# Performance work log

Measured on AMD Instinct MI355X. Metric: run time of the kernel, lower is better.

Reference implementation:

```python
import jax, jax.numpy as jnp
import numpy as np

N = 20000      # nodes
E = 320000     # edges per relation
D = 128        # d_model
H = 2          # attention heads


def _gat(x, src, dst, W, al, ar, b):
    """DGL-style GATConv on a single relation (same src/dst node type).
    x: [N, in], W: [in, H*O], al/ar: [H, O], b: [H*O]. Returns [N, H, O]."""
    h, o = al.shape
    feat = (x @ W).reshape(N, h, o)                 # [N, H, O]
    el = jnp.sum(feat * al, axis=-1)                # [N, H]
    er = jnp.sum(feat * ar, axis=-1)                # [N, H]
    e = jax.nn.leaky_relu(el[src] + er[dst], 0.2)   # [E, H] per-edge logits
    m = jax.ops.segment_max(e, dst, num_segments=N)            # per-dst max
    ee = jnp.exp(e - m[dst])
    s = jax.ops.segment_sum(ee, dst, num_segments=N)
    alpha = ee / jnp.maximum(s[dst], 1e-9)          # edge softmax over incoming edges
    out = jax.ops.segment_sum(alpha[:, :, None] * feat[src], dst, num_segments=N)
    return out + b.reshape(1, h, o)


def setup_inputs() -> dict:
    key = jax.random.key(0)
    ks = jax.random.split(key, 24)
    d = {
        'x': jax.random.normal(ks[0], (N, D), jnp.float32),
        'src0': jax.random.randint(ks[1], (E,), 0, N, jnp.int32),
        'dst0': jax.random.randint(ks[2], (E,), 0, N, jnp.int32),
        'src1': jax.random.randint(ks[3], (E,), 0, N, jnp.int32),
        'dst1': jax.random.randint(ks[4], (E,), 0, N, jnp.int32),
    }
    sc = 0.1
    # layer 1: in=D, out per head=2D, heads=H
    d['W1_0'] = jax.random.normal(ks[5], (D, H * 2 * D), jnp.float32) * sc
    d['al1_0'] = jax.random.normal(ks[6], (H, 2 * D), jnp.float32) * sc
    d['ar1_0'] = jax.random.normal(ks[7], (H, 2 * D), jnp.float32) * sc
    d['b1_0'] = jnp.zeros((H * 2 * D,), jnp.float32)
    d['W1_1'] = jax.random.normal(ks[8], (D, H * 2 * D), jnp.float32) * sc
    d['al1_1'] = jax.random.normal(ks[9], (H, 2 * D), jnp.float32) * sc
    d['ar1_1'] = jax.random.normal(ks[10], (H, 2 * D), jnp.float32) * sc
    d['b1_1'] = jnp.zeros((H * 2 * D,), jnp.float32)
    # layer 2: in=2D, out per head=D, heads=H
    d['W2_0'] = jax.random.normal(ks[11], (2 * D, H * D), jnp.float32) * sc
    d['al2_0'] = jax.random.normal(ks[12], (H, D), jnp.float32) * sc
    d['ar2_0'] = jax.random.normal(ks[13], (H, D), jnp.float32) * sc
    d['b2_0'] = jnp.zeros((H * D,), jnp.float32)
    d['W2_1'] = jax.random.normal(ks[14], (2 * D, H * D), jnp.float32) * sc
    d['al2_1'] = jax.random.normal(ks[15], (H, D), jnp.float32) * sc
    d['ar2_1'] = jax.random.normal(ks[16], (H, D), jnp.float32) * sc
    d['b2_1'] = jnp.zeros((H * D,), jnp.float32)
    return d


def reference(x, src0, dst0, src1, dst1,
              W1_0, al1_0, ar1_0, b1_0, W1_1, al1_1, ar1_1, b1_1,
              W2_0, al2_0, ar2_0, b2_0, W2_1, al2_1, ar2_1, b2_1):
    # conv1: HeteroGraphConv sum over relations, then mean over heads, relu
    h1 = _gat(x, src0, dst0, W1_0, al1_0, ar1_0, b1_0) \
       + _gat(x, src1, dst1, W1_1, al1_1, ar1_1, b1_1)   # [N, H, 2D]
    h1 = jax.nn.relu(h1.mean(axis=1))                    # [N, 2D]; dropout is eval-mode identity
    # conv2: same structure, then mean over heads
    h2 = _gat(h1, src0, dst0, W2_0, al2_0, ar2_0, b2_0) \
       + _gat(h1, src1, dst1, W2_1, al2_1, ar2_1, b2_1)  # [N, H, D]
    return h2.mean(axis=1)                                # [N, D]
```

## Files before the change

kernel.cpp:

```cpp
#include <hip/hip_runtime.h>


#define NN 20000
#define NE 320000

typedef unsigned short bf16_t;
typedef __attribute__((ext_vector_type(8))) short short8;
typedef __attribute__((ext_vector_type(4))) float f32x4;

__device__ __forceinline__ float bf2f(bf16_t u) {
    return __uint_as_float(((unsigned)u) << 16);
}
__device__ __forceinline__ bf16_t f2bf(float f) {
    unsigned x = __float_as_uint(f);
    unsigned r = (x + 0x7fffu + ((x >> 16) & 1u)) >> 16;
    return (bf16_t)r;
}
__device__ __forceinline__ unsigned pk2bf(float a, float b) {
    return (unsigned)f2bf(a) | ((unsigned)f2bf(b) << 16);
}
__device__ __forceinline__ float lrelu(float v) {
    return (v > 0.f) ? v : 0.2f * v;
}
__device__ __forceinline__ void load_x2(const void* x, int flag, int idx,
                                        float& v0, float& v1) {
    if (flag) {
        float2 f = ((const float2*)x)[idx];
        v0 = f.x; v1 = f.y;
    } else {
        unsigned pk = ((const unsigned*)x)[idx];
        v0 = bf2f((bf16_t)(pk & 0xffffu));
        v1 = bf2f((bf16_t)(pk >> 16));
    }
}

#define NTC 16
struct CzArgs {
    const void* src[NTC];
    bf16_t* dst[NTC];
    int n[NTC];
    int nblk[NTC + 1];
    int* zero_ptr;
    int zn;
    const unsigned* xsrc;
    int* flag_out;
};
__global__ void convzero_kernel(CzArgs a) {
    __shared__ int fl_s;
    int t = threadIdx.x;
    if (t < 64) {
        float mx = 0.f;
        for (int i = t; i < 256; i += 64) {
            float v = fabsf(bf2f((bf16_t)(a.xsrc[i] & 0xffffu)));
            v = (v <= 1e30f) ? v : 1e30f;
            mx = fmaxf(mx, v);
        }
        for (int off = 32; off > 0; off >>= 1) mx = fmaxf(mx, __shfl_xor(mx, off));
        if (t == 0) {
            int f = (mx > 1e6f) ? 1 : 0;
            fl_s = f;
            if (blockIdx.x == 0) *a.flag_out = f;
        }
    }
    __syncthreads();
    int flag = fl_s;
    int b = blockIdx.x;
    int ti = 0;
#pragma unroll 1
    for (; ti <= NTC; ++ti) {
        if (b < a.nblk[ti]) break;
        b -= a.nblk[ti];
    }
    int i = b * 256 + t;
    if (ti < NTC) {
        if (i < a.n[ti]) {
            if (flag) a.dst[ti][i] = f2bf(((const float*)a.src[ti])[i]);
            else      a.dst[ti][i] = ((const bf16_t*)a.src[ti])[i];
        }
    } else {
        if (i < a.zn) a.zero_ptr[i] = 0;
    }
}

struct PrepArgs {
    const bf16_t *W1[2], *W2[2];
    const bf16_t *al1[2], *ar1[2], *al2[2], *ar2[2];
    const bf16_t *b1[2], *b2[2];
    float *wal1, *war1;
    float *wal2, *war2;
    float *bc1, *bc2;
    bf16_t *Wc1f;
    bf16_t *Wzf;
};
__device__ __forceinline__ void prep_body(const PrepArgs& p, int bx, int tid) {
    if (bx < 4) {
        int t = bx * 256 + tid;
        int lr = t >> 9, rel = (t >> 8) & 1, h = (t >> 7) & 1, k = t & 127;
        const bf16_t* av = lr ? p.ar1[rel] : p.al1[rel];
        const bf16_t* W = p.W1[rel];
        float s = 0.f;
        for (int o = 0; o < 256; ++o)
            s += bf2f(W[k * 512 + h * 256 + o]) * bf2f(av[h * 256 + o]);
        (lr ? p.war1 : p.wal1)[(rel * 2 + h) * 128 + k] = s;
    } else if (bx < 12) {
        int t = (bx - 4) * 256 + tid;
        int lr = t >> 10, rel = (t >> 9) & 1, h = (t >> 8) & 1, k = t & 255;
        const bf16_t* av = lr ? p.ar2[rel] : p.al2[rel];
        const bf16_t* W = p.W2[rel];
        float s = 0.f;
        for (int o = 0; o < 128; ++o)
            s += bf2f(W[k * 256 + h * 128 + o]) * bf2f(av[h * 128 + o]);
        (lr ? p.war2 : p.wal2)[(rel * 2 + h) * 256 + k] = s;
    } else if (bx < 14) {
        int t = (bx - 12) * 256 + tid;
        if (t < 256) {
            p.bc1[t] = 0.5f * (bf2f(p.b1[0][t]) + bf2f(p.b1[0][256 + t]) +
                               bf2f(p.b1[1][t]) + bf2f(p.b1[1][256 + t]));
        } else if (t < 384) {
            int o = t - 256;
            p.bc2[o] = 0.5f * (bf2f(p.b2[0][o]) + bf2f(p.b2[0][128 + o]) +
                               bf2f(p.b2[1][o]) + bf2f(p.b2[1][128 + o]));
        }
    } else if (bx < 78) {
        int i = (bx - 14) * 256 + tid;
        int lane = i & 63;
        int t2 = i >> 6;
        int ct = t2 >> 4, ks = t2 & 15;
        int col = ct * 16 + (lane & 15);
        bf16_t* out = p.Wc1f + (size_t)i * 8;
#pragma unroll
        for (int j = 0; j < 8; ++j) {
            int r = ks * 32 + ((lane >> 4) << 3) + j;
            int rel = r >> 8, h = (r >> 7) & 1, kx = r & 127;
            out[j] = f2bf(0.5f * bf2f(p.W1[rel][kx * 512 + h * 256 + col]));
        }
    } else {
        int b = bx - 78;
        int rel = b >> 5;
        int i = (b & 31) * 256 + tid;
        int lane = i & 63;
        int t2 = i >> 6;
        int ct = t2 >> 3, ks = t2 & 7;
        int col = ct * 16 + (lane & 15);
        bf16_t* out = p.Wzf + (size_t)rel * 65536 + (size_t)i * 8;
#pragma unroll
        for (int j = 0; j < 8; ++j) {
            int r = ks * 32 + ((lane >> 4) << 3) + j;
            out[j] = f2bf(0.5f * bf2f(p.W2[rel][r * 256 + col]));
        }
    }
}

struct Csr2 {
    const int* src[2];
    const int* dst[2];
    int* cnt[2];
    int* offs[2];
    int* rank[2];
    int* srcc[2];
};
struct PhArgs { PrepArgs p; Csr2 c; };
__global__ void prep_hist_kernel(PhArgs a) {
    int bx = blockIdx.x;
    if (bx < 142) {
        prep_body(a.p, bx, threadIdx.x);
    } else {
        int b = bx - 142;
        int rel = b / 1250;
        int i = (b - rel * 1250) * 256 + threadIdx.x;
        if (i < NE)
            a.c.rank[rel][i] = atomicAdd(&a.c.cnt[rel][a.c.dst[rel][i]], 1);
    }
}

__global__ void scan2_kernel(Csr2 c, int n) {
    int rel = blockIdx.x;
    const int* cnt = c.cnt[rel];
    int* offs = c.offs[rel];
    __shared__ int sums[256];
    int t = threadIdx.x;
    int chunk = (n + 255) >> 8;
    int lo = t * chunk;
    int hi = min(lo + chunk, n);
    int s = 0;
    for (int i = lo; i < hi; ++i) s += cnt[i];
    sums[t] = s;
    __syncthreads();
    if (t == 0) {
        int run = 0;
        for (int i = 0; i < 256; ++i) { int v = sums[i]; sums[i] = run; run += v; }
    }
    __syncthreads();
    int run = sums[t];
    for (int i = lo; i < hi; ++i) { int v = cnt[i]; offs[i] = run; run += v; }
    if (t == 255) offs[n] = run;
}

__global__ void scat_elr_kernel(Csr2 c, const void* __restrict__ x,
                                const int* __restrict__ flagp,
                                const float* __restrict__ wal1,
                                const float* __restrict__ war1,
                                float* __restrict__ el0, float* __restrict__ er0,
                                float* __restrict__ el1, float* __restrict__ er1) {
    __shared__ float wl[512], wr[512];
    int t = threadIdx.x;
    if (blockIdx.x < 5000) {
        wl[t] = wal1[t]; wl[t + 256] = wal1[t + 256];
        wr[t] = war1[t]; wr[t + 256] = war1[t + 256];
        __syncthreads();
        int fl = *flagp;
        int w = t >> 6, lane = t & 63;
        int node = blockIdx.x * 4 + w;
        float v0, v1;
        load_x2(x, fl, node * 64 + lane, v0, v1);
        float de[4], dr[4];
#pragma unroll
        for (int cch = 0; cch < 4; ++cch) {
            de[cch] = v0 * wl[cch * 128 + 2 * lane] + v1 * wl[cch * 128 + 2 * lane + 1];
            dr[cch] = v0 * wr[cch * 128 + 2 * lane] + v1 * wr[cch * 128 + 2 * lane + 1];
        }
#pragma unroll
        for (int off = 32; off > 0; off >>= 1) {
#pragma unroll
            for (int cch = 0; cch < 4; ++cch) {
                de[cch] += __shfl_xor(de[cch], off);
                dr[cch] += __shfl_xor(dr[cch], off);
            }
        }
        if (lane == 0) {
            el0[node * 2 + 0] = de[0]; el0[node * 2 + 1] = de[1];
            el1[node * 2 + 0] = de[2]; el1[node * 2 + 1] = de[3];
            er0[node * 2 + 0] = dr[0]; er0[node * 2 + 1] = dr[1];
            er1[node * 2 + 0] = dr[2]; er1[node * 2 + 1] = dr[3];
        }
    } else {
        int b = blockIdx.x - 5000;
        int rel = b / 313;
        int base = (b - rel * 313) * 1024 + t * 4;
        const int* dstp = c.dst[rel];
        const int* srcp = c.src[rel];
        const int* rkp  = c.rank[rel];
        const int* offp = c.offs[rel];
        int* sc = c.srcc[rel];
        if (base + 3 < NE) {
            int4 dv = *(const int4*)(dstp + base);
            int4 rv = *(const int4*)(rkp + base);
            int4 sv = *(const int4*)(srcp + base);
            sc[offp[dv.x] + rv.x] = sv.x;
            sc[offp[dv.y] + rv.y] = sv.y;
            sc[offp[dv.z] + rv.z] = sv.z;
            sc[offp[dv.w] + rv.w] = sv.w;
        } else {
            for (int k = 0; k < 4 && base + k < NE; ++k)
                sc[offp[dstp[base + k]] + rkp[base + k]] = srcp[base + k];
        }
    }
}

__device__ __forceinline__ void wave_softmax(
    const int* __restrict__ srcc, int beg, int deg,
    const float* __restrict__ el, float er_h0, float er_h1, int lane,
    int& sreg, float& a0, float& a1,
    float& m0, float& i0, float& m1, float& i1) {
    float mm0 = -1e30f, ss0 = 0.f, mm1 = -1e30f, ss1 = 0.f;
    float e0r = 0.f, e1r = 0.f;
    sreg = 0;
    for (int j = lane; j < deg; j += 64) {
        int s = srcc[beg + j];
        float2 ev = ((const float2*)el)[s];
        float e0 = lrelu(ev.x + er_h0);
        float e1 = lrelu(ev.y + er_h1);
        if (j < 64) { sreg = s; e0r = e0; e1r = e1; }
        float mn0 = fmaxf(mm0, e0);
        ss0 = ss0 * __expf(mm0 - mn0) + __expf(e0 - mn0);
        mm0 = mn0;
        float mn1 = fmaxf(mm1, e1);
        ss1 = ss1 * __expf(mm1 - mn1) + __expf(e1 - mn1);
        mm1 = mn1;
    }
#pragma unroll
    for (int off = 1; off < 64; off <<= 1) {
        float om = __shfl_xor(mm0, off), os = __shfl_xor(ss0, off);
        float mn = fmaxf(mm0, om);
        ss0 = ss0 * __expf(mm0 - mn) + os * __expf(om - mn);
        mm0 = mn;
        om = __shfl_xor(mm1, off); os = __shfl_xor(ss1, off);
        mn = fmaxf(mm1, om);
        ss1 = ss1 * __expf(mm1 - mn) + os * __expf(om - mn);
        mm1 = mn;
    }
    m0 = mm0; m1 = mm1;
    i0 = 1.f / fmaxf(ss0, 1e-9f);
    i1 = 1.f / fmaxf(ss1, 1e-9f);
    a0 = __expf(e0r - m0) * i0;
    a1 = __expf(e1r - m1) * i1;
}

__global__ void agg1_kernel(
    const int* __restrict__ offs0, const int* __restrict__ srcc0,
    const float* __restrict__ el0, const float* __restrict__ er0,
    const int* __restrict__ offs1, const int* __restrict__ srcc1,
    const float* __restrict__ el1, const float* __restrict__ er1,
    const void* __restrict__ x, const int* __restrict__ flagp,
    bf16_t* __restrict__ y1) {
    int t = threadIdx.x;
    int w = t >> 6, lane = t & 63;
    int slot = lane >> 5, m = lane & 31;
    int d = blockIdx.x * 4 + w;
    int beg0 = offs0[d], deg0 = offs0[d + 1] - beg0;
    int beg1 = offs1[d], deg1 = offs1[d + 1] - beg1;
    float er00 = er0[d * 2], er01 = er0[d * 2 + 1];
    float er10 = er1[d * 2], er11 = er1[d * 2 + 1];
    int fl = *flagp;

    int sr0, sr1;
    float a00, a01, a10, a11;
    float m00, i00, m01, i01, m10, i10, m11, i11;
    wave_softmax(srcc0, beg0, deg0, el0, er00, er01, lane, sr0, a00, a01, m00, i00, m01, i01);
    wave_softmax(srcc1, beg1, deg1, el1, er10, er11, lane, sr1, a10, a11, m10, i10, m11, i11);

    auto xload = [&](int s, float v[4]) {
        if (fl) {
            float4 f = ((const float4*)x)[s * 32 + m];
            v[0] = f.x; v[1] = f.y; v[2] = f.z; v[3] = f.w;
        } else {
            uint2 pk = ((const uint2*)x)[s * 32 + m];
            v[0] = bf2f((bf16_t)(pk.x & 0xffffu));
            v[1] = bf2f((bf16_t)(pk.x >> 16));
            v[2] = bf2f((bf16_t)(pk.y & 0xffffu));
            v[3] = bf2f((bf16_t)(pk.y >> 16));
        }
    };
    float h0[4] = {}, h1[4] = {};
    float g0[4] = {}, g1[4] = {};
    {
        int dm = min(deg0, 64);
        int T = (dm + 3) & ~3;
        for (int jj = slot; jj < T; jj += 4) {
            int j2 = jj + 2;
            int sA = __shfl(sr0, jj), sB = __shfl(sr0, j2);
            float pA0 = __shfl(a00, jj), pA1 = __shfl(a01, jj);
            float pB0 = __shfl(a00, j2), pB1 = __shfl(a01, j2);
            if (jj >= dm) { sA = 0; pA0 = 0.f; pA1 = 0.f; }
            if (j2 >= dm) { sB = 0; pB0 = 0.f; pB1 = 0.f; }
            float vA[4], vB[4];
            xload(sA, vA);
            xload(sB, vB);
#pragma unroll
            for (int k = 0; k < 4; ++k) {
                h0[k] += pA0 * vA[k] + pB0 * vB[k];
                h1[k] += pA1 * vA[k] + pB1 * vB[k];
            }
        }
        for (int jj = 64 + slot; jj < deg0; jj += 2) {
            int sA = srcc0[beg0 + jj];
            float2 ev = ((const float2*)el0)[sA];
            float pA0 = __expf(lrelu(ev.x + er00) - m00) * i00;
            float pA1 = __expf(lrelu(ev.y + er01) - m01) * i01;
            float vA[4];
            xload(sA, vA);
#pragma unroll
            for (int k = 0; k < 4; ++k) {
                h0[k] += pA0 * vA[k];
                h1[k] += pA1 * vA[k];
            }
        }
    }
    {
        int dm = min(deg1, 64);
        int T = (dm + 3) & ~3;
        for (int jj = slot; jj < T; jj += 4) {
            int j2 = jj + 2;
            int sA = __shfl(sr1, jj), sB = __shfl(sr1, j2);
            float pA0 = __shfl(a10, jj), pA1 = __shfl(a11, jj);
            float pB0 = __shfl(a10, j2), pB1 = __shfl(a11, j2);
            if (jj >= dm) { sA = 0; pA0 = 0.f; pA1 = 0.f; }
            if (j2 >= dm) { sB = 0; pB0 = 0.f; pB1 = 0.f; }
            float vA[4], vB[4];
            xload(sA, vA);
            xload(sB, vB);
#pragma unroll
            for (int k = 0; k < 4; ++k) {
                g0[k] += pA0 * vA[k] + pB0 * vB[k];
                g1[k] += pA1 * vA[k] + pB1 * vB[k];
            }
        }
        for (int jj = 64 + slot; jj < deg1; jj += 2) {
            int sA = srcc1[beg1 + jj];
            float2 ev = ((const float2*)el1)[sA];
            float pA0 = __expf(lrelu(ev.x + er10) - m10) * i10;
            float pA1 = __expf(lrelu(ev.y + er11) - m11) * i11;
            float vA[4];
            xload(sA, vA);
#pragma unroll
            for (int k = 0; k < 4; ++k) {
                g0[k] += pA0 * vA[k];
                g1[k] += pA1 * vA[k];
            }
        }
    }
#pragma unroll
    for (int k = 0; k < 4; ++k) {
        h0[k] += __shfl_xor(h0[k], 32);
        h1[k] += __shfl_xor(h1[k], 32);
        g0[k] += __shfl_xor(g0[k], 32);
        g1[k] += __shfl_xor(g1[k], 32);
    }
    if (slot == 0) {
        bf16_t* yr = y1 + (size_t)d * 512;
        uint2 u;
        u.x = pk2bf(h0[0], h0[1]); u.y = pk2bf(h0[2], h0[3]);
        ((uint2*)yr)[m] = u;
        u.x = pk2bf(h1[0], h1[1]); u.y = pk2bf(h1[2], h1[3]);
        ((uint2*)(yr + 128))[m] = u;
        u.x = pk2bf(g0[0], g0[1]); u.y = pk2bf(g0[2], g0[3]);
        ((uint2*)(yr + 256))[m] = u;
        u.x = pk2bf(g1[0], g1[1]); u.y = pk2bf(g1[2], g1[3]);
        ((uint2*)(yr + 384))[m] = u;
    }
}

__global__ void gemm1_kernel(const bf16_t* __restrict__ A, const bf16_t* __restrict__ Wf,
                             const float* __restrict__ bc1, bf16_t* __restrict__ h1,
                             const float* __restrict__ wal2, const float* __restrict__ war2,
                             float* __restrict__ el2_0, float* __restrict__ er2_0,
                             float* __restrict__ el2_1, float* __restrict__ er2_1,
                             int n) {
    constexpr int K = 512, M = 256, KS = 16, NF = 8;
    int w = threadIdx.x >> 6, lane = threadIdx.x & 63;
    int q = lane >> 4, m16 = lane & 15;
    int rf = blockIdx.y * 64 + w * 16;
    if (rf >= n) return;
    f32x4 acc[NF] = {};
    const bf16_t* Arow = A + (size_t)(rf + m16) * K + q * 8;
    for (int ks = 0; ks < KS; ++ks) {
        short8 af = *(const short8*)(Arow + ks * 32);
#pragma unroll
        for (int f = 0; f < NF; ++f) {
            int ct = blockIdx.x * NF + f;
            short8 bfr = *(const short8*)(Wf + ((size_t)(ct * KS + ks) * 64 + lane) * 8);
            acc[f] = __builtin_amdgcn_mfma_f32_16x16x32_bf16(af, bfr, acc[f], 0, 0, 0);
        }
    }
    int col0 = blockIdx.x * (NF * 16);
    float del[2][2][4] = {};
    float der[2][2][4] = {};
#pragma unroll
    for (int f = 0; f < NF; ++f) {
        int col = col0 + f * 16 + m16;
        float bcv = bc1[col];
        float wle[2][2], wre[2][2];
#pragma unroll
        for (int rel = 0; rel < 2; ++rel)
#pragma unroll
            for (int h = 0; h < 2; ++h) {
                wle[rel][h] = wal2[(rel * 2 + h) * 256 + col];
                wre[rel][h] = war2[(rel * 2 + h) * 256 + col];
            }
#pragma unroll
        for (int r = 0; r < 4; ++r) {
            int row = rf + q * 4 + r;
            float v = fmaxf(acc[f][r] + bcv, 0.f);
            bf16_t hb = f2bf(v);
            h1[(size_t)row * M + col] = hb;
            float vb = bf2f(hb);
#pragma unroll
            for (int rel = 0; rel < 2; ++rel)
#pragma unroll
                for (int h = 0; h < 2; ++h) {
                    del[rel][h][r] += vb * wle[rel][h];
                    der[rel][h][r] += vb * wre[rel][h];
                }
        }
    }
#pragma unroll
    for (int off = 1; off < 16; off <<= 1) {
#pragma unroll
        for (int rel = 0; rel < 2; ++rel)
#pragma unroll
            for (int h = 0; h < 2; ++h)
#pragma unroll
                for (int r = 0; r < 4; ++r) {
                    del[rel][h][r] += __shfl_xor(del[rel][h][r], off);
                    der[rel][h][r] += __shfl_xor(der[rel][h][r], off);
                }
    }
    if (m16 == 0) {
#pragma unroll
        for (int r = 0; r < 4; ++r) {
            int row = rf + q * 4 + r;
            atomicAdd(&el2_0[row * 2 + 0], del[0][0][r]);
            atomicAdd(&el2_0[row * 2 + 1], del[0][1][r]);
            atomicAdd(&el2_1[row * 2 + 0], del[1][0][r]);
            atomicAdd(&el2_1[row * 2 + 1], del[1][1][r]);
            atomicAdd(&er2_0[row * 2 + 0], der[0][0][r]);
            atomicAdd(&er2_0[row * 2 + 1], der[0][1][r]);
            atomicAdd(&er2_1[row * 2 + 0], der[1][0][r]);
            atomicAdd(&er2_1[row * 2 + 1], der[1][1][r]);
        }
    }
}

__global__ void gemmz_kernel(const bf16_t* __restrict__ A, const bf16_t* __restrict__ Wzf,
                             bf16_t* __restrict__ z, int n) {
    constexpr int K = 256, M = 256, KS = 8, NF = 8;
    int rel = blockIdx.z;
    const bf16_t* Wf = Wzf + (size_t)rel * 65536;
    bf16_t* C = z + (size_t)rel * NN * 256;
    int w = threadIdx.x >> 6, lane = threadIdx.x & 63;
    int q = lane >> 4, m16 = lane & 15;
    int rf = blockIdx.y * 64 + w * 16;
    if (rf >= n) return;
    f32x4 acc[NF] = {};
    const bf16_t* Arow = A + (size_t)(rf + m16) * K + q * 8;
    for (int ks = 0; ks < KS; ++ks) {
        short8 af = *(const short8*)(Arow + ks * 32);
#pragma unroll
        for (int f = 0; f < NF; ++f) {
            int ct = blockIdx.x * NF + f;
            short8 bfr = *(const short8*)(Wf + ((size_t)(ct * KS + ks) * 64 + lane) * 8);
            acc[f] = __builtin_amdgcn_mfma_f32_16x16x32_bf16(af, bfr, acc[f], 0, 0, 0);
        }
    }
    int col0 = blockIdx.x * (NF * 16);
#pragma unroll
    for (int f = 0; f < NF; ++f) {
#pragma unroll
        for (int r = 0; r < 4; ++r) {
            int row = rf + q * 4 + r;
            C[(size_t)row * M + col0 + f * 16 + m16] = f2bf(acc[f][r]);
        }
    }
}

__global__ void aggout_kernel(
    const int* __restrict__ offs0, const int* __restrict__ srcc0,
    const float* __restrict__ el0, const float* __restrict__ er0,
    const int* __restrict__ offs1, const int* __restrict__ srcc1,
    const float* __restrict__ el1, const float* __restrict__ er1,
    const bf16_t* __restrict__ z, const float* __restrict__ bc2,
    void* __restrict__ out, const int* __restrict__ flagp) {
    int t = threadIdx.x;
    int w = t >> 6, lane = t & 63;
    int slot = lane >> 5, m = lane & 31;
    int h = m >> 4;
    int d = blockIdx.x * 4 + w;
    int beg0 = offs0[d], deg0 = offs0[d + 1] - beg0;
    int beg1 = offs1[d], deg1 = offs1[d + 1] - beg1;
    float er00 = er0[d * 2], er01 = er0[d * 2 + 1];
    float er10 = er1[d * 2], er11 = er1[d * 2 + 1];

    int sr0, sr1;
    float a00, a01, a10, a11;
    float m00, i00, m01, i01, m10, i10, m11, i11;
    wave_softmax(srcc0, beg0, deg0, el0, er00, er01, lane, sr0, a00, a01, m00, i00, m01, i01);
    wave_softmax(srcc1, beg1, deg1, el1, er10, er11, lane, sr1, a10, a11, m10, i10, m11, i11);

    float acc[8] = {};
    auto fmadd8 = [&](float a, uint4 p) {
        acc[0] += a * bf2f((bf16_t)(p.x & 0xffffu));
        acc[1] += a * bf2f((bf16_t)(p.x >> 16));
        acc[2] += a * bf2f((bf16_t)(p.y & 0xffffu));
        acc[3] += a * bf2f((bf16_t)(p.y >> 16));
        acc[4] += a * bf2f((bf16_t)(p.z & 0xffffu));
        acc[5] += a * bf2f((bf16_t)(p.z >> 16));
        acc[6] += a * bf2f((bf16_t)(p.w & 0xffffu));
        acc[7] += a * bf2f((bf16_t)(p.w >> 16));
    };
    {
        const uint4* zp = (const uint4*)z;
        int dm = min(deg0, 64);
        int T = (dm + 3) & ~3;
        for (int jj = slot; jj < T; jj += 4) {
            int j2 = jj + 2;
            int sA = __shfl(sr0, jj), sB = __shfl(sr0, j2);
            float xA0 = __shfl(a00, jj), xA1 = __shfl(a01, jj);
            float xB0 = __shfl(a00, j2), xB1 = __shfl(a01, j2);
            float aA = h ? xA1 : xA0;
            float aB = h ? xB1 : xB0;
            if (jj >= dm) { sA = 0; aA = 0.f; }
            if (j2 >= dm) { sB = 0; aB = 0.f; }
            uint4 pA = zp[sA * 32 + m];
            uint4 pB = zp[sB * 32 + m];
            fmadd8(aA, pA);
            fmadd8(aB, pB);
        }
        for (int jj = 64 + slot; jj < deg0; jj += 2) {
            int sA = srcc0[beg0 + jj];
            float2 ev = ((const float2*)el0)[sA];
            float aA = h ? (__expf(lrelu(ev.y + er01) - m01) * i01)
                         : (__expf(lrelu(ev.x + er00) - m00) * i00);
            uint4 pA = zp[sA * 32 + m];
            fmadd8(aA, pA);
        }
    }
    {
        const uint4* zp = (const uint4*)(z + (size_t)NN * 256);
        int dm = min(deg1, 64);
        int T = (dm + 3) & ~3;
        for (int jj = slot; jj < T; jj += 4) {
            int j2 = jj + 2;
            int sA = __shfl(sr1, jj), sB = __shfl(sr1, j2);
            float xA0 = __shfl(a10, jj), xA1 = __shfl(a11, jj);
            float xB0 = __shfl(a10, j2), xB1 = __shfl(a11, j2);
            float aA = h ? xA1 : xA0;
            float aB = h ? xB1 : xB0;
            if (jj >= dm) { sA = 0; aA = 0.f; }
            if (j2 >= dm) { sB = 0; aB = 0.f; }
            uint4 pA = zp[sA * 32 + m];
            uint4 pB = zp[sB * 32 + m];
            fmadd8(aA, pA);
            fmadd8(aB, pB);
        }
        for (int jj = 64 + slot; jj < deg1; jj += 2) {
            int sA = srcc1[beg1 + jj];
            float2 ev = ((const float2*)el1)[sA];
            float aA = h ? (__expf(lrelu(ev.y + er11) - m11) * i11)
                         : (__expf(lrelu(ev.x + er10) - m10) * i10);
            uint4 pA = zp[sA * 32 + m];
            fmadd8(aA, pA);
        }
    }
#pragma unroll
    for (int k = 0; k < 8; ++k) acc[k] += __shfl_xor(acc[k], 32);
#pragma unroll
    for (int k = 0; k < 8; ++k) acc[k] += __shfl_xor(acc[k], 16);
    if (slot == 0 && m < 16) {
        float4 b0 = ((const float4*)bc2)[m * 2];
        float4 b1 = ((const float4*)bc2)[m * 2 + 1];
        float o0 = acc[0] + b0.x, o1 = acc[1] + b0.y;
        float o2 = acc[2] + b0.z, o3 = acc[3] + b0.w;
        float o4 = acc[4] + b1.x, o5 = acc[5] + b1.y;
        float o6 = acc[6] + b1.z, o7 = acc[7] + b1.w;
        if (*flagp) {
            float4* op = (float4*)out + (size_t)d * 32 + m * 2;
            op[0] = make_float4(o0, o1, o2, o3);
            op[1] = make_float4(o4, o5, o6, o7);
        } else {
            uint4 u;
            u.x = pk2bf(o0, o1); u.y = pk2bf(o2, o3);
            u.z = pk2bf(o4, o5); u.w = pk2bf(o6, o7);
            ((uint4*)out)[(size_t)d * 16 + m] = u;
        }
    }
}

extern "C" void kernel_launch(void* const* d_in, const int* in_sizes, int n_in,
                              void* d_out, int out_size, void* d_ws, size_t ws_size,
                              hipStream_t stream) {
    (void)in_sizes; (void)n_in; (void)out_size; (void)ws_size;
    const void* x0 = d_in[0];
    const int* src0 = (const int*)d_in[1];
    const int* dst0 = (const int*)d_in[2];
    const int* src1 = (const int*)d_in[3];
    const int* dst1 = (const int*)d_in[4];

    char* ws = (char*)d_ws;
    size_t off = 0;
    auto alloc = [&](size_t bytes) -> void* {
        void* p = ws + off;
        off = (off + bytes + 255) & ~(size_t)255;
        return p;
    };
    int* flag = (int*)alloc(4);
    static const int tn[NTC] = {128 * 512, 512, 512, 512,
                                128 * 512, 512, 512, 512,
                                256 * 256, 256, 256, 256,
                                256 * 256, 256, 256, 256};
    bf16_t* tb[NTC];
    for (int i = 0; i < NTC; ++i) tb[i] = (bf16_t*)alloc((size_t)tn[i] * 2);

    bf16_t* Wc1f = (bf16_t*)alloc((size_t)512 * 256 * 2);
    bf16_t* Wzf  = (bf16_t*)alloc((size_t)2 * 65536 * 2);
    float* wal1 = (float*)alloc(512 * 4);
    float* war1 = (float*)alloc(512 * 4);
    float* wal2 = (float*)alloc(1024 * 4);
    float* war2 = (float*)alloc(1024 * 4);
    float* bc1  = (float*)alloc(256 * 4);
    float* bc2  = (float*)alloc(128 * 4);

    char* zbeg = ws + off;
    int* cnt0 = (int*)alloc(NN * 4);
    int* cnt1 = (int*)alloc(NN * 4);
    float* el2_0 = (float*)alloc(NN * 2 * 4);
    float* er2_0 = (float*)alloc(NN * 2 * 4);
    float* el2_1 = (float*)alloc(NN * 2 * 4);
    float* er2_1 = (float*)alloc(NN * 2 * 4);
    char* zend = ws + off;
    int zcount = (int)((zend - zbeg) >> 2);

    int* offs0 = (int*)alloc((NN + 1) * 4);
    int* offs1 = (int*)alloc((NN + 1) * 4);
    int* rank0 = (int*)alloc(NE * 4);
    int* rank1 = (int*)alloc(NE * 4);
    int* srcc0 = (int*)alloc(NE * 4);
    int* srcc1 = (int*)alloc(NE * 4);
    float* el1_0 = (float*)alloc(NN * 2 * 4);
    float* er1_0 = (float*)alloc(NN * 2 * 4);
    float* el1_1 = (float*)alloc(NN * 2 * 4);
    float* er1_1 = (float*)alloc(NN * 2 * 4);
    bf16_t* h1 = (bf16_t*)alloc((size_t)NN * 256 * 2);
    bf16_t* Y  = (bf16_t*)alloc((size_t)NN * 1024 * 2);
    bf16_t* y1 = Y;
    bf16_t* z  = Y;

    CzArgs cz;
    static const int din_idx[NTC] = {5, 6, 7, 8, 9, 10, 11, 12,
                                     13, 14, 15, 16, 17, 18, 19, 20};
    int total_blocks = 0;
    for (int i = 0; i < NTC; ++i) {
        cz.src[i] = d_in[din_idx[i]];
        cz.dst[i] = tb[i];
        cz.n[i] = tn[i];
        cz.nblk[i] = (tn[i] + 255) / 256;
        total_blocks += cz.nblk[i];
    }
    cz.zero_ptr = (int*)zbeg;
    cz.zn = zcount;
    cz.nblk[NTC] = (zcount + 255) / 256;
    total_blocks += cz.nblk[NTC];
    cz.xsrc = (const unsigned*)x0;
    cz.flag_out = flag;
    convzero_kernel<<<total_blocks, 256, 0, stream>>>(cz);

    PhArgs ph;
    ph.p.W1[0] = tb[0];  ph.p.W1[1] = tb[4];
    ph.p.W2[0] = tb[8];  ph.p.W2[1] = tb[12];
    ph.p.al1[0] = tb[1]; ph.p.ar1[0] = tb[2];
    ph.p.al1[1] = tb[5]; ph.p.ar1[1] = tb[6];
    ph.p.al2[0] = tb[9]; ph.p.ar2[0] = tb[10];
    ph.p.al2[1] = tb[13]; ph.p.ar2[1] = tb[14];
    ph.p.b1[0] = tb[3];  ph.p.b1[1] = tb[7];
    ph.p.b2[0] = tb[11]; ph.p.b2[1] = tb[15];
    ph.p.wal1 = wal1; ph.p.war1 = war1;
    ph.p.wal2 = wal2; ph.p.war2 = war2;
    ph.p.bc1 = bc1; ph.p.bc2 = bc2;
    ph.p.Wc1f = Wc1f; ph.p.Wzf = Wzf;
    ph.c.src[0] = src0; ph.c.src[1] = src1;
    ph.c.dst[0] = dst0; ph.c.dst[1] = dst1;
    ph.c.cnt[0] = cnt0; ph.c.cnt[1] = cnt1;
    ph.c.offs[0] = offs0; ph.c.offs[1] = offs1;
    ph.c.rank[0] = rank0; ph.c.rank[1] = rank1;
    ph.c.srcc[0] = srcc0; ph.c.srcc[1] = srcc1;
    prep_hist_kernel<<<142 + 2500, 256, 0, stream>>>(ph);

    scan2_kernel<<<2, 256, 0, stream>>>(ph.c, NN);

    scat_elr_kernel<<<5000 + 626, 256, 0, stream>>>(
        ph.c, x0, flag, wal1, war1, el1_0, er1_0, el1_1, er1_1);

    agg1_kernel<<<5000, 256, 0, stream>>>(offs0, srcc0, el1_0, er1_0,
                                          offs1, srcc1, el1_1, er1_1, x0, flag, y1);

    gemm1_kernel<<<dim3(2, 313), 256, 0, stream>>>(
        y1, Wc1f, bc1, h1, wal2, war2, el2_0, er2_0, el2_1, er2_1, NN);

    gemmz_kernel<<<dim3(2, 313, 2), 256, 0, stream>>>(h1, Wzf, z, NN);

    aggout_kernel<<<5000, 256, 0, stream>>>(offs0, srcc0, el2_0, er2_0,
                                            offs1, srcc1, el2_1, er2_1,
                                            z, bc2, d_out, flag);
}
```

Baseline: 323.1 us.

## Split per-node aggregation across relations into separate waves

In both aggregation kernels, each wave now handles one (node, relation) pair instead of one node covering both relations. The grids double, so there are twice as many waves and each runs a shorter serial chain of softmax and gather loops. In aggout the two relation partial sums are combined through shared memory with a block barrier before the bias add and store. This trades extra shared-memory traffic and a sync for more parallelism and latency hiding, and the duplicated per-relation code goes away.

```diff
diff --git a/kernel.cpp b/kernel.cpp
--- a/kernel.cpp
+++ b/kernel.cpp
@@ -306,18 +306,19 @@
     int t = threadIdx.x;
     int w = t >> 6, lane = t & 63;
     int slot = lane >> 5, m = lane & 31;
-    int d = blockIdx.x * 4 + w;
-    int beg0 = offs0[d], deg0 = offs0[d + 1] - beg0;
-    int beg1 = offs1[d], deg1 = offs1[d + 1] - beg1;
-    float er00 = er0[d * 2], er01 = er0[d * 2 + 1];
-    float er10 = er1[d * 2], er11 = er1[d * 2 + 1];
+    int d = blockIdx.x * 2 + (w >> 1);
+    int rel = w & 1;
+    const int* offs = rel ? offs1 : offs0;
+    const int* srcc = rel ? srcc1 : srcc0;
+    const float* el = rel ? el1 : el0;
+    const float* er = rel ? er1 : er0;
+    int beg = offs[d], deg = offs[d + 1] - beg;
+    float erh0 = er[d * 2], erh1 = er[d * 2 + 1];
     int fl = *flagp;
 
-    int sr0, sr1;
-    float a00, a01, a10, a11;
-    float m00, i00, m01, i01, m10, i10, m11, i11;
-    wave_softmax(srcc0, beg0, deg0, el0, er00, er01, lane, sr0, a00, a01, m00, i00, m01, i01);
-    wave_softmax(srcc1, beg1, deg1, el1, er10, er11, lane, sr1, a10, a11, m10, i10, m11, i11);
+    int sr;
+    float a0, a1, m0, i0, m1, i1;
+    wave_softmax(srcc, beg, deg, el, erh0, erh1, lane, sr, a0, a1, m0, i0, m1, i1);
 
     auto xload = [&](int s, float v[4]) {
         if (fl) {
@@ -332,15 +333,14 @@
         }
     };
     float h0[4] = {}, h1[4] = {};
-    float g0[4] = {}, g1[4] = {};
     {
-        int dm = min(deg0, 64);
+        int dm = min(deg, 64);
         int T = (dm + 3) & ~3;
         for (int jj = slot; jj < T; jj += 4) {
             int j2 = jj + 2;
-            int sA = __shfl(sr0, jj), sB = __shfl(sr0, j2);
-            float pA0 = __shfl(a00, jj), pA1 = __shfl(a01, jj);
-            float pB0 = __shfl(a00, j2), pB1 = __shfl(a01, j2);
+            int sA = __shfl(sr, jj), sB = __shfl(sr, j2);
+            float pA0 = __shfl(a0, jj), pA1 = __shfl(a1, jj);
+            float pB0 = __shfl(a0, j2), pB1 = __shfl(a1, j2);
             if (jj >= dm) { sA = 0; pA0 = 0.f; pA1 = 0.f; }
             if (j2 >= dm) { sB = 0; pB0 = 0.f; pB1 = 0.f; }
             float vA[4], vB[4];
@@ -352,11 +352,11 @@
                 h1[k] += pA1 * vA[k] + pB1 * vB[k];
             }
         }
-        for (int jj = 64 + slot; jj < deg0; jj += 2) {
-            int sA = srcc0[beg0 + jj];
-            float2 ev = ((const float2*)el0)[sA];
-            float pA0 = __expf(lrelu(ev.x + er00) - m00) * i00;
-            float pA1 = __expf(lrelu(ev.y + er01) - m01) * i01;
+        for (int jj = 64 + slot; jj < deg; jj += 2) {
+            int sA = srcc[beg + jj];
+            float2 ev = ((const float2*)el)[sA];
+            float pA0 = __expf(lrelu(ev.x + erh0) - m0) * i0;
+            float pA1 = __expf(lrelu(ev.y + erh1) - m1) * i1;
             float vA[4];
             xload(sA, vA);
 #pragma unroll
@@ -366,57 +366,18 @@
             }
         }
     }
-    {
-        int dm = min(deg1, 64);
-        int T = (dm + 3) & ~3;
-        for (int jj = slot; jj < T; jj += 4) {
-            int j2 = jj + 2;
-            int sA = __shfl(sr1, jj), sB = __shfl(sr1, j2);
-            float pA0 = __shfl(a10, jj), pA1 = __shfl(a11, jj);
-            float pB0 = __shfl(a10, j2), pB1 = __shfl(a11, j2);
-            if (jj >= dm) { sA = 0; pA0 = 0.f; pA1 = 0.f; }
-            if (j2 >= dm) { sB = 0; pB0 = 0.f; pB1 = 0.f; }
-            float vA[4], vB[4];
-            xload(sA, vA);
-            xload(sB, vB);
-#pragma unroll
-            for (int k = 0; k < 4; ++k) {
-                g0[k] += pA0 * vA[k] + pB0 * vB[k];
-                g1[k] += pA1 * vA[k] + pB1 * vB[k];
-            }
-        }
-        for (int jj = 64 + slot; jj < deg1; jj += 2) {
-            int sA = srcc1[beg1 + jj];
-            float2 ev = ((const float2*)el1)[sA];
-            float pA0 = __expf(lrelu(ev.x + er10) - m10) * i10;
-            float pA1 = __expf(lrelu(ev.y + er11) - m11) * i11;
-            float vA[4];
-            xload(sA, vA);
-#pragma unroll
-            for (int k = 0; k < 4; ++k) {
-                g0[k] += pA0 * vA[k];
-                g1[k] += pA1 * vA[k];
-            }
-        }
-    }
 #pragma unroll
     for (int k = 0; k < 4; ++k) {
         h0[k] += __shfl_xor(h0[k], 32);
         h1[k] += __shfl_xor(h1[k], 32);
-        g0[k] += __shfl_xor(g0[k], 32);
-        g1[k] += __shfl_xor(g1[k], 32);
     }
     if (slot == 0) {
-        bf16_t* yr = y1 + (size_t)d * 512;
+        bf16_t* yr = y1 + (size_t)d * 512 + rel * 256;
         uint2 u;
         u.x = pk2bf(h0[0], h0[1]); u.y = pk2bf(h0[2], h0[3]);
         ((uint2*)yr)[m] = u;
         u.x = pk2bf(h1[0], h1[1]); u.y = pk2bf(h1[2], h1[3]);
         ((uint2*)(yr + 128))[m] = u;
-        u.x = pk2bf(g0[0], g0[1]); u.y = pk2bf(g0[2], g0[3]);
-        ((uint2*)(yr + 256))[m] = u;
-        u.x = pk2bf(g1[0], g1[1]); u.y = pk2bf(g1[2], g1[3]);
-        ((uint2*)(yr + 384))[m] = u;
     }
 }
 
@@ -540,21 +501,23 @@
     const float* __restrict__ el1, const float* __restrict__ er1,
     const bf16_t* __restrict__ z, const float* __restrict__ bc2,
     void* __restrict__ out, const int* __restrict__ flagp) {
+    __shared__ float sh[4][128];
     int t = threadIdx.x;
     int w = t >> 6, lane = t & 63;
     int slot = lane >> 5, m = lane & 31;
     int h = m >> 4;
-    int d = blockIdx.x * 4 + w;
-    int beg0 = offs0[d], deg0 = offs0[d + 1] - beg0;
-    int beg1 = offs1[d], deg1 = offs1[d + 1] - beg1;
-    float er00 = er0[d * 2], er01 = er0[d * 2 + 1];
-    float er10 = er1[d * 2], er11 = er1[d * 2 + 1];
-
-    int sr0, sr1;
-    float a00, a01, a10, a11;
-    float m00, i00, m01, i01, m10, i10, m11, i11;
-    wave_softmax(srcc0, beg0, deg0, el0, er00, er01, lane, sr0, a00, a01, m00, i00, m01, i01);
-    wave_softmax(srcc1, beg1, deg1, el1, er10, er11, lane, sr1, a10, a11, m10, i10, m11, i11);
+    int d = blockIdx.x * 2 + (w >> 1);
+    int rel = w & 1;
+    const int* offs = rel ? offs1 : offs0;
+    const int* srcc = rel ? srcc1 : srcc0;
+    const float* el = rel ? el1 : el0;
+    const float* er = rel ? er1 : er0;
+    int beg = offs[d], deg = offs[d + 1] - beg;
+    float erh0 = er[d * 2], erh1 = er[d * 2 + 1];
+
+    int sr;
+    float a0, a1, m0, i0, m1, i1;
+    wave_softmax(srcc, beg, deg, el, erh0, erh1, lane, sr, a0, a1, m0, i0, m1, i1);
 
     float acc[8] = {};
     auto fmadd8 = [&](float a, uint4 p) {
@@ -568,14 +531,14 @@
         acc[7] += a * bf2f((bf16_t)(p.w >> 16));
     };
     {
-        const uint4* zp = (const uint4*)z;
-        int dm = min(deg0, 64);
+        const uint4* zp = (const uint4*)(z + (size_t)rel * NN * 256);
+        int dm = min(deg, 64);
         int T = (dm + 3) & ~3;
         for (int jj = slot; jj < T; jj += 4) {
             int j2 = jj + 2;
-            int sA = __shfl(sr0, jj), sB = __shfl(sr0, j2);
-            float xA0 = __shfl(a00, jj), xA1 = __shfl(a01, jj);
-            float xB0 = __shfl(a00, j2), xB1 = __shfl(a01, j2);
+            int sA = __shfl(sr, jj), sB = __shfl(sr, j2);
+            float xA0 = __shfl(a0, jj), xA1 = __shfl(a1, jj);
+            float xB0 = __shfl(a0, j2), xB1 = __shfl(a1, j2);
             float aA = h ? xA1 : xA0;
             float aB = h ? xB1 : xB0;
             if (jj >= dm) { sA = 0; aA = 0.f; }
@@ -585,64 +548,30 @@
             fmadd8(aA, pA);
             fmadd8(aB, pB);
         }
-        for (int jj = 64 + slot; jj < deg0; jj += 2) {
-            int sA = srcc0[beg0 + jj];
-            float2 ev = ((const float2*)el0)[sA];
-            float aA = h ? (__expf(lrelu(ev.y + er01) - m01) * i01)
-                         : (__expf(lrelu(ev.x + er00) - m00) * i00);
+        for (int jj = 64 + slot; jj < deg; jj += 2) {
+            int sA = srcc[beg + jj];
+            float2 ev = ((const float2*)el)[sA];
+            float aA = h ? (__expf(lrelu(ev.y + erh1) - m1) * i1)
+                         : (__expf(lrelu(ev.x + erh0) - m0) * i0);
             uint4 pA = zp[sA * 32 + m];
             fmadd8(aA, pA);
         }
     }
-    {
-        const uint4* zp = (const uint4*)(z + (size_t)NN * 256);
-        int dm = min(deg1, 64);
-        int T = (dm + 3) & ~3;
-        for (int jj = slot; jj < T; jj += 4) {
-            int j2 = jj + 2;
-            int sA = __shfl(sr1, jj), sB = __shfl(sr1, j2);
-            float xA0 = __shfl(a10, jj), xA1 = __shfl(a11, jj);
-            float xB0 = __shfl(a10, j2), xB1 = __shfl(a11, j2);
-            float aA = h ? xA1 : xA0;
-            float aB = h ? xB1 : xB0;
-            if (jj >= dm) { sA = 0; aA = 0.f; }
-            if (j2 >= dm) { sB = 0; aB = 0.f; }
-            uint4 pA = zp[sA * 32 + m];
-            uint4 pB = zp[sB * 32 + m];
-            fmadd8(aA, pA);
-            fmadd8(aB, pB);
-        }
-        for (int jj = 64 + slot; jj < deg1; jj += 2) {
-            int sA = srcc1[beg1 + jj];
-            float2 ev = ((const float2*)el1)[sA];
-            float aA = h ? (__expf(lrelu(ev.y + er11) - m11) * i11)
-                         : (__expf(lrelu(ev.x + er10) - m10) * i10);
-            uint4 pA = zp[sA * 32 + m];
-            fmadd8(aA, pA);
-        }
-    }
 #pragma unroll
     for (int k = 0; k < 8; ++k) acc[k] += __shfl_xor(acc[k], 32);
 #pragma unroll
     for (int k = 0; k < 8; ++k) acc[k] += __shfl_xor(acc[k], 16);
     if (slot == 0 && m < 16) {
-        float4 b0 = ((const float4*)bc2)[m * 2];
-        float4 b1 = ((const float4*)bc2)[m * 2 + 1];
-        float o0 = acc[0] + b0.x, o1 = acc[1] + b0.y;
-        float o2 = acc[2] + b0.z, o3 = acc[3] + b0.w;
-        float o4 = acc[4] + b1.x, o5 = acc[5] + b1.y;
-        float o6 = acc[6] + b1.z, o7 = acc[7] + b1.w;
-        if (*flagp) {
-            float4* op = (float4*)out + (size_t)d * 32 + m * 2;
-            op[0] = make_float4(o0, o1, o2, o3);
-            op[1] = make_float4(o4, o5, o6, o7);
-        } else {
-            uint4 u;
-            u.x = pk2bf(o0, o1); u.y = pk2bf(o2, o3);
-            u.z = pk2bf(o4, o5); u.w = pk2bf(o6, o7);
-            ((uint4*)out)[(size_t)d * 16 + m] = u;
-        }
-    }
+#pragma unroll
+        for (int k = 0; k < 8; ++k) sh[w][m * 8 + k] = acc[k];
+    }
+    __syncthreads();
+    int ni = t >> 7;
+    int o = t & 127;
+    int dd = blockIdx.x * 2 + ni;
+    float v = bc2[o] + sh[ni * 2][o] + sh[ni * 2 + 1][o];
+    if (*flagp) ((float*)out)[(size_t)dd * 128 + o] = v;
+    else        ((bf16_t*)out)[(size_t)dd * 128 + o] = f2bf(v);
 }
 
 extern "C" void kernel_launch(void* const* d_in, const int* in_sizes, int n_in,
@@ -749,15 +678,15 @@
     scat_elr_kernel<<<5000 + 626, 256, 0, stream>>>(
         ph.c, x0, flag, wal1, war1, el1_0, er1_0, el1_1, er1_1);
 
-    agg1_kernel<<<5000, 256, 0, stream>>>(offs0, srcc0, el1_0, er1_0,
-                                          offs1, srcc1, el1_1, er1_1, x0, flag, y1);
+    agg1_kernel<<<10000, 256, 0, stream>>>(offs0, srcc0, el1_0, er1_0,
+                                           offs1, srcc1, el1_1, er1_1, x0, flag, y1);
 
     gemm1_kernel<<<dim3(2, 313), 256, 0, stream>>>(
         y1, Wc1f, bc1, h1, wal2, war2, el2_0, er2_0, el2_1, er2_1, NN);
 
     gemmz_kernel<<<dim3(2, 313, 2), 256, 0, stream>>>(h1, Wzf, z, NN);
 
-    aggout_kernel<<<5000, 256, 0, stream>>>(offs0, srcc0, el2_0, er2_0,
-                                            offs1, srcc1, el2_1, er2_1,
-                                            z, bc2, d_out, flag);
-}
+    aggout_kernel<<<10000, 256, 0, stream>>>(offs0, srcc0, el2_0, er2_0,
+                                             offs1, srcc1, el2_1, er2_1,
+                                             z, bc2, d_out, flag);
+}
```

Result: no change. 325.1 us (+0.6%).
